# Kernel optimization log

Measured on AMD Instinct MI355X. Metric: run time of the kernel, lower is better.

## Reference

```python
import jax, jax.numpy as jnp
import numpy as np

DIM = 1024
TOPK = 64
PAIRS = DIM // 2  # phase_pairs default
PHASE_MIX = 0.5
GATE_THRESHOLD = 0.0
EPS = 1e-12  # F.normalize default eps


def _l2norm(v):
    # matches F.normalize(v, dim=-1): v / max(||v||, eps)
    n = jnp.linalg.norm(v, axis=-1, keepdims=True)
    return v / jnp.maximum(n, EPS)


def setup_inputs() -> dict:
    key = jax.random.key(0)
    ks = jax.random.split(key, 6)
    s = 0.02  # small init scale for weights
    return {
        "x": jax.random.normal(ks[0], (4, 4096, DIM), dtype=jnp.float32),
        "gate_W": jax.random.normal(ks[1], (DIM, DIM), dtype=jnp.float32) * s,
        "gate_b": jnp.zeros((DIM,), dtype=jnp.float32),
        "mag_W": jax.random.normal(ks[2], (DIM, DIM), dtype=jnp.float32) * s,
        "mag_b": jnp.zeros((DIM,), dtype=jnp.float32),
        "Wq": jax.random.normal(ks[3], (DIM, DIM), dtype=jnp.float32) * s,
        "Wk": jax.random.normal(ks[4], (DIM, DIM), dtype=jnp.float32) * s,
        "phase_W": jax.random.normal(ks[5], (2 * PAIRS, DIM), dtype=jnp.float32) * s,
    }


def reference(x, gate_W, gate_b, mag_W, mag_b, Wq, Wk, phase_W):
    B, S, D = x.shape
    # gated SAE-style projection (gated=True, diag=False)
    gate_pre = x @ gate_W.T + gate_b          # [B,S,D]
    mag_pre = x @ mag_W.T + mag_b             # [B,S,D]
    # hard gate with straight-through estimator
    gate_soft = jax.nn.sigmoid(gate_pre)
    gate_hard = (gate_pre > GATE_THRESHOLD).astype(x.dtype)
    gate = gate_hard + gate_soft - jax.lax.stop_gradient(gate_soft)
    mag = jax.nn.relu(mag_pre)
    # top-k scatter mask along feature dim
    idx = jax.lax.top_k(gate_pre, TOPK)[1]    # [B,S,K]
    rows = jnp.arange(B * S)[:, None]
    mask = (jnp.zeros((B * S, D), dtype=bool)
            .at[rows, idx.reshape(B * S, TOPK)].set(True)
            .reshape(B, S, D))
    gate = jnp.where(mask, gate, jnp.zeros_like(gate))
    mag = jnp.where(mask, mag, jnp.zeros_like(mag))
    xg = gate * mag
    # twist projections, L2-normalized
    q = _l2norm(xg @ Wq.T)
    k = _l2norm(xg @ Wk.T)
    # symplectic momentum map over consecutive steps
    momentum_map = q[:, 1:] * k[:, :-1] - q[:, :-1] * k[:, 1:]  # [B,S-1,D]
    twist_mag = jnp.linalg.norm(momentum_map, axis=-1, keepdims=True)
    complexity = jnp.pad(jnp.tanh(twist_mag), ((0, 0), (1, 0), (0, 0)))  # [B,S,1]
    # phase branch (phase_mix > 0)
    phase = (xg @ phase_W.T).reshape(B, S, PAIRS, 2)
    phase = _l2norm(phase)
    pp, pc = phase[:, :-1], phase[:, 1:]
    cross = pp[..., 0] * pc[..., 1] - pp[..., 1] * pc[..., 0]   # [B,S-1,P]
    dot = jnp.clip(jnp.sum(pp * pc, axis=-1), -1.0, 1.0)
    phase_delta = jnp.abs(jnp.arctan2(cross, dot)) / jnp.pi
    phase_score = jnp.pad(jnp.mean(phase_delta, axis=-1, keepdims=True),
                          ((0, 0), (1, 0), (0, 0)))             # [B,S,1]
    return (1.0 - PHASE_MIX) * complexity + PHASE_MIX * phase_score
```

## Files before the change

kernel.cpp:

```cpp
#include <hip/hip_runtime.h>
#include <math.h>

#define DIM 1024
#define ROWS 16384
#define SEQ 4096
#define MARGIN 0.012f
#define MAXC 24

typedef __bf16 v8bf __attribute__((ext_vector_type(8)));
typedef float v4f __attribute__((ext_vector_type(4)));

__device__ __forceinline__ unsigned short f2bf(float f){
  unsigned u = __float_as_uint(f);
  u = u + 0x7FFFu + ((u >> 16) & 1u);
  return (unsigned short)(u >> 16);
}
__device__ __forceinline__ float bf2f(unsigned short h){
  return __uint_as_float(((unsigned)h) << 16);
}
__device__ __forceinline__ unsigned short relu_bf(unsigned short h){
  return (h & 0x8000u) ? (unsigned short)0 : h;
}
__device__ __forceinline__ void lds_fence(){
  __asm__ volatile("s_waitcnt lgkmcnt(0)" ::: "memory");
}

__global__ __launch_bounds__(256) void cvt_all(
    const float* __restrict__ x,
    const float* __restrict__ w0, const float* __restrict__ w1,
    const float* __restrict__ w2, const float* __restrict__ w3,
    const float* __restrict__ w4,
    unsigned short* __restrict__ xbf, unsigned short* __restrict__ wbf){
  const int y = blockIdx.y;
  const float* s;
  unsigned short* d;
  if (y < 16){ s = x + ((size_t)y << 20); d = xbf + ((size_t)y << 20); }
  else {
    const float* srcs[5] = {w0, w1, w2, w3, w4};
    s = srcs[y - 16]; d = wbf + ((size_t)(y - 16) << 20);
  }
  int i = (blockIdx.x * 256 + threadIdx.x) * 4;
  float4 f = *(const float4*)(s + i);
  ushort4 o;
  o.x = f2bf(f.x); o.y = f2bf(f.y); o.z = f2bf(f.z); o.w = f2bf(f.w);
  *(ushort4*)(d + i) = o;
}

__global__ __launch_bounds__(256, 4) void gemm_bt(
    const unsigned short* __restrict__ A, const unsigned short* __restrict__ B,
    const float* __restrict__ bias0, const float* __restrict__ bias1,
    void* __restrict__ C0, void* __restrict__ C1, void* __restrict__ C2,
    int bf16mask)
{
  __shared__ unsigned short lA[128 * 32];
  __shared__ unsigned short lB[128 * 32];
  const int t = threadIdx.x;
  const int lane = t & 63, wave = t >> 6;
  const int bid = blockIdx.y * gridDim.x + blockIdx.x;
  const int m0 = (bid & 127) * 128;
  const int n0 = (bid >> 7) * 128;
  const int wm = (wave >> 1) * 64, wn = (wave & 1) * 64;
  const int ar = lane & 15, aq = lane >> 4;

  v4f acc[4][4];
#pragma unroll
  for (int i = 0; i < 4; i++)
#pragma unroll
    for (int j = 0; j < 4; j++) acc[i][j] = v4f{0.f, 0.f, 0.f, 0.f};

  for (int k0 = 0; k0 < DIM; k0 += 32){
#pragma unroll
    for (int i = 0; i < 2; i++){
      int c = (wave * 2 + i) * 64 + lane;
      int row = c >> 2, kq = c & 3;
      __builtin_amdgcn_global_load_lds(
        (const __attribute__((address_space(1))) void*)(A + (size_t)(m0 + row) * DIM + k0 + kq * 8),
        (__attribute__((address_space(3))) void*)(&lA[c * 8]), 16, 0, 0);
      __builtin_amdgcn_global_load_lds(
        (const __attribute__((address_space(1))) void*)(B + (size_t)(n0 + row) * DIM + k0 + kq * 8),
        (__attribute__((address_space(3))) void*)(&lB[c * 8]), 16, 0, 0);
    }
    __syncthreads();
    v8bf af[4], bf[4];
#pragma unroll
    for (int i = 0; i < 4; i++){
      af[i] = *(const v8bf*)&lA[(wm + i * 16 + ar) * 32 + aq * 8];
      bf[i] = *(const v8bf*)&lB[(wn + i * 16 + ar) * 32 + aq * 8];
    }
#pragma unroll
    for (int mi = 0; mi < 4; mi++)
#pragma unroll
      for (int ni = 0; ni < 4; ni++)
        acc[mi][ni] = __builtin_amdgcn_mfma_f32_16x16x32_bf16(af[mi], bf[ni], acc[mi][ni], 0, 0, 0);
    __syncthreads();
  }

  const int os = n0 >> 10;
  void* Cp = (os == 0) ? C0 : ((os == 1) ? C1 : C2);
  const float* bp = (os == 0) ? bias0 : ((os == 1) ? bias1 : nullptr);
  const bool half_out = ((bf16mask >> os) & 1) != 0;
#pragma unroll
  for (int mi = 0; mi < 4; mi++)
#pragma unroll
    for (int ni = 0; ni < 4; ni++){
      int col = (n0 + wn + ni * 16 + ar) & (DIM - 1);
      float bv = bp ? bp[col] : 0.f;
#pragma unroll
      for (int rr = 0; rr < 4; rr++){
        int rowg = m0 + wm + mi * 16 + aq * 4 + rr;
        float val = acc[mi][ni][rr] + bv;
        if (half_out) ((unsigned short*)Cp)[(size_t)rowg * DIM + col] = f2bf(val);
        else          ((float*)Cp)[(size_t)rowg * DIM + col] = val;
      }
    }
}

__global__ __launch_bounds__(256) void select_k(
  const unsigned short* __restrict__ gate_pre, const unsigned short* __restrict__ mag_pre,
  const float* __restrict__ x, const float* __restrict__ gW, const float* __restrict__ gb,
  unsigned short* __restrict__ xg)
{
  __shared__ int   s_cnt[4];
  __shared__ int   s_idx[4][MAXC];
  __shared__ float s_ex [4][MAXC];
  __shared__ int   s_res[4][MAXC];

  const int t = threadIdx.x;
  const int lane = t & 63, wave = t >> 6;
  const int r = blockIdx.x * 4 + wave;
  const size_t rb = (size_t)r * DIM;

  float vg[16], vx[16];
  unsigned short mg[16];
#pragma unroll
  for (int c = 0; c < 4; c++){
    ushort4 g4 = *(const ushort4*)(gate_pre + rb + c * 256 + lane * 4);
    float4 x4 = *(const float4*)(x          + rb + c * 256 + lane * 4);
    ushort4 m4 = *(const ushort4*)(mag_pre  + rb + c * 256 + lane * 4);
    vg[c*4+0]=bf2f(g4.x); vg[c*4+1]=bf2f(g4.y); vg[c*4+2]=bf2f(g4.z); vg[c*4+3]=bf2f(g4.w);
    vx[c*4+0]=x4.x; vx[c*4+1]=x4.y; vx[c*4+2]=x4.z; vx[c*4+3]=x4.w;
    mg[c*4+0]=m4.x; mg[c*4+1]=m4.y; mg[c*4+2]=m4.z; mg[c*4+3]=m4.w;
  }
  if (lane == 0) s_cnt[wave] = 0;

  float lo = -8.f, hi = 8.f;
#pragma unroll
  for (int it = 0; it < 15; it++){
    float mid = 0.5f * (lo + hi);
    int cn = 0;
#pragma unroll
    for (int e = 0; e < 16; e++) cn += (vg[e] > mid) ? 1 : 0;
#pragma unroll
    for (int m = 32; m; m >>= 1) cn += __shfl_xor(cn, m);
    if (cn >= 64) lo = mid; else hi = mid;
  }
  const float cl = lo - MARGIN, ch = hi + MARGIN;

  int n1 = 0;
#pragma unroll
  for (int e = 0; e < 16; e++) n1 += (vg[e] > ch) ? 1 : 0;
#pragma unroll
  for (int m = 32; m; m >>= 1) n1 += __shfl_xor(n1, m);
  const int s = 64 - n1;

  lds_fence();
#pragma unroll
  for (int e = 0; e < 16; e++){
    float vv = vg[e];
    if (vv >= cl && vv <= ch){
      int p = atomicAdd(&s_cnt[wave], 1);
      if (p < MAXC) s_idx[wave][p] = (e >> 2) * 256 + lane * 4 + (e & 3);
    }
  }
  lds_fence();
  int namb = s_cnt[wave]; if (namb > MAXC) namb = MAXC;

  for (int i = 0; i < namb; i++){
    int d = s_idx[wave][i];
    const float* wr = gW + (size_t)d * DIM;
    float p = 0.f;
#pragma unroll
    for (int c = 0; c < 4; c++){
      float4 w4 = *(const float4*)(wr + c * 256 + lane * 4);
      p = fmaf(vx[c*4+0], w4.x, p); p = fmaf(vx[c*4+1], w4.y, p);
      p = fmaf(vx[c*4+2], w4.z, p); p = fmaf(vx[c*4+3], w4.w, p);
    }
#pragma unroll
    for (int m = 32; m; m >>= 1) p += __shfl_xor(p, m);
    if (lane == 0) s_ex[wave][i] = p + gb[d];
  }
  lds_fence();

  if (lane < namb){
    float e = s_ex[wave][lane]; int d = s_idx[wave][lane];
    int rank = 0;
    for (int j = 0; j < namb; j++){
      float ej = s_ex[wave][j]; int dj = s_idx[wave][j];
      if (ej > e || (ej == e && dj < d)) rank++;
    }
    s_res[wave][lane] = (rank < s && e > 0.f) ? 1 : 0;
  }
  lds_fence();

  unsigned short o16[16];
#pragma unroll
  for (int e = 0; e < 16; e++)
    o16[e] = (vg[e] > ch) ? ((vg[e] > 0.f) ? relu_bf(mg[e]) : (unsigned short)0)
                          : (unsigned short)0;
  for (int i = 0; i < namb; i++){
    int d = s_idx[wave][i];
    int res = s_res[wave][i];
    if (((d >> 2) & 63) == lane){
      int e = (d >> 8) * 4 + (d & 3);
      o16[e] = res ? relu_bf(mg[e]) : (unsigned short)0;
    }
  }
#pragma unroll
  for (int c = 0; c < 4; c++){
    ushort4 o; o.x = o16[c*4+0]; o.y = o16[c*4+1]; o.z = o16[c*4+2]; o.w = o16[c*4+3];
    *(ushort4*)(xg + rb + c * 256 + lane * 4) = o;
  }
}

__global__ __launch_bounds__(256) void epilogue_k(
  const unsigned short* __restrict__ q_pre, const unsigned short* __restrict__ k_pre,
  const unsigned short* __restrict__ p_pre, float* __restrict__ out)
{
  const int r0 = blockIdx.x * 4;
  const int t = threadIdx.x;
  const int lane = t & 63, wave = t >> 6;
  __shared__ float red[16];

  const int rp = (r0 == 0) ? 0 : r0 - 1;
  float vqp[4], vkp[4], vpp[4];
  {
    ushort4 uq = *(const ushort4*)(q_pre + (size_t)rp * DIM + 4*t);
    ushort4 uk = *(const ushort4*)(k_pre + (size_t)rp * DIM + 4*t);
    ushort4 up = *(const ushort4*)(p_pre + (size_t)rp * DIM + 4*t);
    vqp[0]=bf2f(uq.x); vqp[1]=bf2f(uq.y); vqp[2]=bf2f(uq.z); vqp[3]=bf2f(uq.w);
    vkp[0]=bf2f(uk.x); vkp[1]=bf2f(uk.y); vkp[2]=bf2f(uk.z); vkp[3]=bf2f(uk.w);
    vpp[0]=bf2f(up.x); vpp[1]=bf2f(up.y); vpp[2]=bf2f(up.z); vpp[3]=bf2f(up.w);
  }
  float aq = 0.f, ak = 0.f;
#pragma unroll
  for (int j = 0; j < 4; j++){ aq = fmaf(vqp[j], vqp[j], aq); ak = fmaf(vkp[j], vkp[j], ak); }
#pragma unroll
  for (int m = 32; m; m >>= 1){ aq += __shfl_xor(aq, m); ak += __shfl_xor(ak, m); }
  if (lane == 0){ red[wave] = aq; red[4 + wave] = ak; }
  __syncthreads();
  float rqp = 1.f / fmaxf(sqrtf(red[0] + red[1] + red[2] + red[3]), 1e-12f);
  float rkp = 1.f / fmaxf(sqrtf(red[4] + red[5] + red[6] + red[7]), 1e-12f);
  __syncthreads();

  for (int rr = 0; rr < 4; rr++){
    const int r = r0 + rr;
    float vqc[4], vkc[4], vpc[4];
    {
      ushort4 uq = *(const ushort4*)(q_pre + (size_t)r * DIM + 4*t);
      ushort4 uk = *(const ushort4*)(k_pre + (size_t)r * DIM + 4*t);
      ushort4 up = *(const ushort4*)(p_pre + (size_t)r * DIM + 4*t);
      vqc[0]=bf2f(uq.x); vqc[1]=bf2f(uq.y); vqc[2]=bf2f(uq.z); vqc[3]=bf2f(uq.w);
      vkc[0]=bf2f(uk.x); vkc[1]=bf2f(uk.y); vkc[2]=bf2f(uk.z); vkc[3]=bf2f(uk.w);
      vpc[0]=bf2f(up.x); vpc[1]=bf2f(up.y); vpc[2]=bf2f(up.z); vpc[3]=bf2f(up.w);
    }
    const bool seg = (r & (SEQ - 1)) == 0;
    float aqc = 0.f, akc = 0.f;
#pragma unroll
    for (int j = 0; j < 4; j++){ aqc = fmaf(vqc[j], vqc[j], aqc); akc = fmaf(vkc[j], vkc[j], akc); }
    float dsum = 0.f;
    if (!seg){
#pragma unroll
      for (int j = 0; j < 2; j++){
        float ax = vpp[2*j], ay = vpp[2*j+1], bx = vpc[2*j], by = vpc[2*j+1];
        float ia = 1.f / fmaxf(sqrtf(ax * ax + ay * ay), 1e-12f);
        float ib = 1.f / fmaxf(sqrtf(bx * bx + by * by), 1e-12f);
        ax *= ia; ay *= ia; bx *= ib; by *= ib;
        float cross = ax * by - ay * bx;
        float dot = fminf(fmaxf(ax * bx + ay * by, -1.f), 1.f);
        dsum += fabsf(atan2f(cross, dot)) * 0.3183098861837907f;
      }
    }
#pragma unroll
    for (int m = 32; m; m >>= 1){
      aqc += __shfl_xor(aqc, m); akc += __shfl_xor(akc, m); dsum += __shfl_xor(dsum, m);
    }
    if (lane == 0){ red[wave] = aqc; red[4 + wave] = akc; red[8 + wave] = dsum; }
    __syncthreads();
    float rqc = 1.f / fmaxf(sqrtf(red[0] + red[1] + red[2] + red[3]), 1e-12f);
    float rkc = 1.f / fmaxf(sqrtf(red[4] + red[5] + red[6] + red[7]), 1e-12f);
    if (!seg){
      float tw = 0.f;
#pragma unroll
      for (int j = 0; j < 4; j++){
        float m = (vqc[j] * rqc) * (vkp[j] * rkp) - (vqp[j] * rqp) * (vkc[j] * rkc);
        tw = fmaf(m, m, tw);
      }
#pragma unroll
      for (int m = 32; m; m >>= 1) tw += __shfl_xor(tw, m);
      if (lane == 0) red[12 + wave] = tw;
      __syncthreads();
      if (t == 0){
        float dtot = red[8] + red[9] + red[10] + red[11];
        float twt = red[12] + red[13] + red[14] + red[15];
        out[r] = 0.5f * tanhf(sqrtf(twt)) + 0.5f * (dtot * (1.f / 512.f));
      }
    } else {
      if (t == 0) out[r] = 0.f;
    }
    __syncthreads();
#pragma unroll
    for (int j = 0; j < 4; j++){ vqp[j] = vqc[j]; vkp[j] = vkc[j]; vpp[j] = vpc[j]; }
    rqp = rqc; rkp = rkc;
  }
}

extern "C" void kernel_launch(void* const* d_in, const int* in_sizes, int n_in,
                              void* d_out, int out_size, void* d_ws, size_t ws_size,
                              hipStream_t stream)
{
  const float* x       = (const float*)d_in[0];
  const float* gate_W  = (const float*)d_in[1];
  const float* gate_b  = (const float*)d_in[2];
  const float* mag_W   = (const float*)d_in[3];
  const float* mag_b   = (const float*)d_in[4];
  const float* Wq      = (const float*)d_in[5];
  const float* Wk      = (const float*)d_in[6];
  const float* phase_W = (const float*)d_in[7];
  float* out = (float*)d_out;

  char* ws = (char*)d_ws;
  unsigned short* xbf = (unsigned short*)ws;
  unsigned short* wbf = (unsigned short*)(ws + 33554432);
  unsigned short* gate_pre = (unsigned short*)(ws + 46137344);
  unsigned short* mag_pre  = (unsigned short*)(ws + 79691776);
  unsigned short* p_pre    = (unsigned short*)(ws + 113246208);
  unsigned short* q_pre = gate_pre;
  unsigned short* k_pre = mag_pre;

  dim3 b256(256);
  cvt_all<<<dim3(1024, 21), b256, 0, stream>>>(x, gate_W, mag_W, Wq, Wk, phase_W, xbf, wbf);

  gemm_bt<<<dim3(16, 128), b256, 0, stream>>>(xbf, wbf, gate_b, mag_b,
                                              gate_pre, mag_pre, nullptr, 0b011);

  unsigned short* xg = xbf;
  select_k<<<ROWS / 4, b256, 0, stream>>>(gate_pre, mag_pre, x, gate_W, gate_b, xg);

  gemm_bt<<<dim3(24, 128), b256, 0, stream>>>(xg, wbf + (2u << 20), nullptr, nullptr,
                                              q_pre, k_pre, p_pre, 0b111);

  epilogue_k<<<ROWS / 4, b256, 0, stream>>>(q_pre, k_pre, p_pre, out);
}
```

Baseline: 425.1 us.

## Run second projection GEMM in FP8 with scaled MFMA

Quantizes the sparse gated activations and the Wq/Wk/phase weights to FP8 e4m3 (weights pre-scaled by 32) and runs the second GEMM with the 16x16x128 scaled f8f6f4 MFMA instead of the bf16 path. This halves operand bytes and targets higher matrix throughput for the largest GEMM. The new kernel uses global_load_lds into LDS tiles with 128-wide K steps and no double buffering, and rescales on output. It risks accuracy loss in the normalized q/k/phase outputs and possible LDS bank conflicts from the unswizzled layout.

```diff
diff --git a/kernel.cpp b/kernel.cpp
--- a/kernel.cpp
+++ b/kernel.cpp
@@ -9,6 +9,7 @@
 
 typedef __bf16 v8bf __attribute__((ext_vector_type(8)));
 typedef float v4f __attribute__((ext_vector_type(4)));
+typedef int v8i __attribute__((ext_vector_type(8)));
 
 __device__ __forceinline__ unsigned short f2bf(float f){
   unsigned u = __float_as_uint(f);
@@ -20,6 +21,22 @@
 }
 __device__ __forceinline__ unsigned short relu_bf(unsigned short h){
   return (h & 0x8000u) ? (unsigned short)0 : h;
+}
+__device__ __forceinline__ unsigned f2fp8(float f){
+  float a = fabsf(f);
+  unsigned sign = (__float_as_uint(f) >> 24) & 0x80u;
+  if (a >= 448.f) return sign | 0x7Eu;
+  if (a < 0.015625f){
+    int k = (int)rintf(a * 512.f);
+    if (k >= 8) return sign | 0x08u;
+    return sign | (unsigned)k;
+  }
+  unsigned u = __float_as_uint(a);
+  u += 0x7FFFFu + ((u >> 20) & 1u);
+  int e = (int)((u >> 23) & 0xFFu) - 127;
+  unsigned m = (u >> 20) & 7u;
+  if (e > 8) return sign | 0x7Eu;
+  return sign | ((unsigned)(e + 7) << 3) | m;
 }
 __device__ __forceinline__ void lds_fence(){
   __asm__ volatile("s_waitcnt lgkmcnt(0)" ::: "memory");
@@ -30,20 +47,27 @@
     const float* __restrict__ w0, const float* __restrict__ w1,
     const float* __restrict__ w2, const float* __restrict__ w3,
     const float* __restrict__ w4,
-    unsigned short* __restrict__ xbf, unsigned short* __restrict__ wbf){
+    unsigned short* __restrict__ xbf, unsigned short* __restrict__ wbf,
+    unsigned char* __restrict__ wf8){
   const int y = blockIdx.y;
-  const float* s;
-  unsigned short* d;
-  if (y < 16){ s = x + ((size_t)y << 20); d = xbf + ((size_t)y << 20); }
-  else {
-    const float* srcs[5] = {w0, w1, w2, w3, w4};
-    s = srcs[y - 16]; d = wbf + ((size_t)(y - 16) << 20);
-  }
   int i = (blockIdx.x * 256 + threadIdx.x) * 4;
-  float4 f = *(const float4*)(s + i);
-  ushort4 o;
-  o.x = f2bf(f.x); o.y = f2bf(f.y); o.z = f2bf(f.z); o.w = f2bf(f.w);
-  *(ushort4*)(d + i) = o;
+  if (y < 16){
+    const float* s = x + ((size_t)y << 20);
+    float4 f = *(const float4*)(s + i);
+    ushort4 o; o.x = f2bf(f.x); o.y = f2bf(f.y); o.z = f2bf(f.z); o.w = f2bf(f.w);
+    *(ushort4*)(xbf + ((size_t)y << 20) + i) = o;
+  } else if (y < 18){
+    const float* s = (y == 16) ? w0 : w1;
+    float4 f = *(const float4*)(s + i);
+    ushort4 o; o.x = f2bf(f.x); o.y = f2bf(f.y); o.z = f2bf(f.z); o.w = f2bf(f.w);
+    *(ushort4*)(wbf + ((size_t)(y - 16) << 20) + i) = o;
+  } else {
+    const float* s = (y == 18) ? w2 : ((y == 19) ? w3 : w4);
+    float4 f = *(const float4*)(s + i);
+    unsigned u = f2fp8(f.x * 32.f) | (f2fp8(f.y * 32.f) << 8) |
+                 (f2fp8(f.z * 32.f) << 16) | (f2fp8(f.w * 32.f) << 24);
+    *(unsigned*)(wf8 + ((size_t)(y - 18) << 20) + i) = u;
+  }
 }
 
 __global__ __launch_bounds__(256, 4) void gemm_bt(
@@ -115,10 +139,74 @@
     }
 }
 
+__global__ __launch_bounds__(256, 3) void gemm8(
+    const unsigned char* __restrict__ A, const unsigned char* __restrict__ B,
+    unsigned short* __restrict__ C0, unsigned short* __restrict__ C1,
+    unsigned short* __restrict__ C2)
+{
+  __shared__ unsigned char lA[128 * 128];
+  __shared__ unsigned char lB[128 * 128];
+  const int t = threadIdx.x;
+  const int lane = t & 63, wave = t >> 6;
+  const int bid = blockIdx.y * gridDim.x + blockIdx.x;
+  const int m0 = (bid & 127) * 128;
+  const int n0 = (bid >> 7) * 128;
+  const int wm = (wave >> 1) * 64, wn = (wave & 1) * 64;
+  const int ar = lane & 15, aq = lane >> 4;
+
+  v4f acc[4][4];
+#pragma unroll
+  for (int i = 0; i < 4; i++)
+#pragma unroll
+    for (int j = 0; j < 4; j++) acc[i][j] = v4f{0.f, 0.f, 0.f, 0.f};
+
+  for (int k0 = 0; k0 < DIM; k0 += 128){
+#pragma unroll
+    for (int i = 0; i < 4; i++){
+      int c = (wave * 4 + i) * 64 + lane;
+      int row = c >> 3, kq = c & 7;
+      __builtin_amdgcn_global_load_lds(
+        (const __attribute__((address_space(1))) void*)(A + (size_t)(m0 + row) * DIM + k0 + kq * 16),
+        (__attribute__((address_space(3))) void*)(&lA[c * 16]), 16, 0, 0);
+      __builtin_amdgcn_global_load_lds(
+        (const __attribute__((address_space(1))) void*)(B + (size_t)(n0 + row) * DIM + k0 + kq * 16),
+        (__attribute__((address_space(3))) void*)(&lB[c * 16]), 16, 0, 0);
+    }
+    __syncthreads();
+    v8i a8[4], b8[4];
+#pragma unroll
+    for (int i = 0; i < 4; i++){
+      a8[i] = *(const v8i*)&lA[(wm + i * 16 + ar) * 128 + aq * 32];
+      b8[i] = *(const v8i*)&lB[(wn + i * 16 + ar) * 128 + aq * 32];
+    }
+#pragma unroll
+    for (int mi = 0; mi < 4; mi++)
+#pragma unroll
+      for (int ni = 0; ni < 4; ni++)
+        acc[mi][ni] = __builtin_amdgcn_mfma_scale_f32_16x16x128_f8f6f4(
+            a8[mi], b8[ni], acc[mi][ni], 0, 0, 0, 127u, 0, 127u);
+    __syncthreads();
+  }
+
+  const int os = n0 >> 10;
+  unsigned short* Cp = (os == 0) ? C0 : ((os == 1) ? C1 : C2);
+#pragma unroll
+  for (int mi = 0; mi < 4; mi++)
+#pragma unroll
+    for (int ni = 0; ni < 4; ni++){
+      int col = (n0 + wn + ni * 16 + ar) & (DIM - 1);
+#pragma unroll
+      for (int rr = 0; rr < 4; rr++){
+        int rowg = m0 + wm + mi * 16 + aq * 4 + rr;
+        Cp[(size_t)rowg * DIM + col] = f2bf(acc[mi][ni][rr] * 0.03125f);
+      }
+    }
+}
+
 __global__ __launch_bounds__(256) void select_k(
   const unsigned short* __restrict__ gate_pre, const unsigned short* __restrict__ mag_pre,
   const float* __restrict__ x, const float* __restrict__ gW, const float* __restrict__ gb,
-  unsigned short* __restrict__ xg)
+  unsigned char* __restrict__ xg8)
 {
   __shared__ int   s_cnt[4];
   __shared__ int   s_idx[4][MAXC];
@@ -202,23 +290,23 @@
   }
   lds_fence();
 
-  unsigned short o16[16];
+  float vals[16];
 #pragma unroll
   for (int e = 0; e < 16; e++)
-    o16[e] = (vg[e] > ch) ? ((vg[e] > 0.f) ? relu_bf(mg[e]) : (unsigned short)0)
-                          : (unsigned short)0;
+    vals[e] = (vg[e] > ch && vg[e] > 0.f) ? bf2f(relu_bf(mg[e])) : 0.f;
   for (int i = 0; i < namb; i++){
     int d = s_idx[wave][i];
     int res = s_res[wave][i];
     if (((d >> 2) & 63) == lane){
       int e = (d >> 8) * 4 + (d & 3);
-      o16[e] = res ? relu_bf(mg[e]) : (unsigned short)0;
+      vals[e] = res ? bf2f(relu_bf(mg[e])) : 0.f;
     }
   }
 #pragma unroll
   for (int c = 0; c < 4; c++){
-    ushort4 o; o.x = o16[c*4+0]; o.y = o16[c*4+1]; o.z = o16[c*4+2]; o.w = o16[c*4+3];
-    *(ushort4*)(xg + rb + c * 256 + lane * 4) = o;
+    unsigned u = f2fp8(vals[c*4+0]) | (f2fp8(vals[c*4+1]) << 8) |
+                 (f2fp8(vals[c*4+2]) << 16) | (f2fp8(vals[c*4+3]) << 24);
+    *(unsigned*)(xg8 + rb + c * 256 + lane * 4) = u;
   }
 }
 
@@ -331,23 +419,24 @@
   char* ws = (char*)d_ws;
   unsigned short* xbf = (unsigned short*)ws;
   unsigned short* wbf = (unsigned short*)(ws + 33554432);
-  unsigned short* gate_pre = (unsigned short*)(ws + 46137344);
-  unsigned short* mag_pre  = (unsigned short*)(ws + 79691776);
-  unsigned short* p_pre    = (unsigned short*)(ws + 113246208);
+  unsigned char*  wf8 = (unsigned char*)(ws + 37748736);
+  unsigned short* gate_pre = (unsigned short*)(ws + 41943040);
+  unsigned short* mag_pre  = (unsigned short*)(ws + 75497472);
+  unsigned short* p_pre    = (unsigned short*)(ws + 109051904);
   unsigned short* q_pre = gate_pre;
   unsigned short* k_pre = mag_pre;
 
   dim3 b256(256);
-  cvt_all<<<dim3(1024, 21), b256, 0, stream>>>(x, gate_W, mag_W, Wq, Wk, phase_W, xbf, wbf);
+  cvt_all<<<dim3(1024, 21), b256, 0, stream>>>(x, gate_W, mag_W, Wq, Wk, phase_W,
+                                               xbf, wbf, wf8);
 
   gemm_bt<<<dim3(16, 128), b256, 0, stream>>>(xbf, wbf, gate_b, mag_b,
                                               gate_pre, mag_pre, nullptr, 0b011);
 
-  unsigned short* xg = xbf;
-  select_k<<<ROWS / 4, b256, 0, stream>>>(gate_pre, mag_pre, x, gate_W, gate_b, xg);
-
-  gemm_bt<<<dim3(24, 128), b256, 0, stream>>>(xg, wbf + (2u << 20), nullptr, nullptr,
-                                              q_pre, k_pre, p_pre, 0b111);
+  unsigned char* xg8 = (unsigned char*)xbf;
+  select_k<<<ROWS / 4, b256, 0, stream>>>(gate_pre, mag_pre, x, gate_W, gate_b, xg8);
+
+  gemm8<<<dim3(24, 128), b256, 0, stream>>>(xg8, wf8, q_pre, k_pre, p_pre);
 
   epilogue_k<<<ROWS / 4, b256, 0, stream>>>(q_pre, k_pre, p_pre, out);
 }
```

Result: faster. 392.7 us (-7.6%).
